# Optimization experiments

Measured on AMD Instinct MI355X. Metric: run time of the kernel, lower is better.

The kernel has to match this reference:

```python
import jax, jax.numpy as jnp
import numpy as np

B, C, T = 8, 128, 8192
SIGMA_MIN = 1e-6

def setup_inputs() -> dict:
    key = jax.random.key(0)
    ks = jax.random.split(key, 9)
    x1 = jax.random.normal(ks[0], (B, C, T), dtype=jnp.float32)
    mu = jax.random.normal(ks[1], (B, C, T), dtype=jnp.float32)
    style = jax.random.normal(ks[2], (B, 192), dtype=jnp.float32)
    t_sample = jax.random.uniform(ks[3], (B, 1, 1), dtype=jnp.float32)
    z = jax.random.normal(ks[4], (B, C, T), dtype=jnp.float32)
    W = jax.random.normal(ks[5], (C, C), dtype=jnp.float32) * (1.0 / np.sqrt(C))
    b_lin = jax.random.normal(ks[6], (C,), dtype=jnp.float32) * 0.01
    prompt_lens = jax.random.randint(ks[7], (B,), 64, T // 4)
    x_lens = jax.random.randint(ks[8], (B,), T // 2, T)
    return {"x1": x1, "mu": mu, "style": style, "t_sample": t_sample, "z": z,
            "W": W, "b_lin": b_lin, "x_lens": x_lens, "prompt_lens": prompt_lens}

def reference(x1, mu, style, t_sample, z, W, b_lin, x_lens, prompt_lens):
    # x1, z: [B, C, T]; t_sample: [B, 1, 1]
    sigma = SIGMA_MIN
    Bb, Cc, Tt = x1.shape
    tpos = jnp.arange(Tt)
    pmask = tpos[None, :] < prompt_lens[:, None]            # [B, T] prompt region
    # flow-matching interpolation
    y = (1.0 - (1.0 - sigma) * t_sample) * z + t_sample * x1
    u = x1 - (1.0 - sigma) * z
    # zero out prompt region of y (prompt copy tensor is unused by the mock estimator)
    y = jnp.where(pmask[:, None, :], 0.0, y)
    # mock estimator: per-timestep Linear over channels
    out = jnp.einsum('bct,dc->bdt', y, W) + b_lin[None, :, None]
    # per-sample MSE over [prompt_lens, x_lens) across all channels, then mean over batch
    lmask = (~pmask) & (tpos[None, :] < x_lens[:, None])     # [B, T]
    diff2 = jnp.square(out - u) * lmask[:, None, :]
    counts = (Cc * jnp.sum(lmask, axis=1)).astype(x1.dtype)  # [B]
    loss = jnp.mean(jnp.sum(diff2, axis=(1, 2)) / counts)
    return loss, out + (1.0 - sigma) * z
```

## Files before the change

kernel.cpp:

```cpp
#include <hip/hip_runtime.h>
#include <hip/hip_bf16.h>

#define BB    8
#define CC    128
#define TLEN  8192
#define TT    32
#define TSPAN 128
#define NB    (BB * (TLEN / TSPAN))

typedef __attribute__((ext_vector_type(8))) short short8;
typedef __attribute__((ext_vector_type(4))) float f32x4;

__device__ __forceinline__ short f2bf(float f) {
    union { float f; unsigned u; } v; v.f = f;
    return (short)((v.u + 0x7FFFu + ((v.u >> 16) & 1u)) >> 16);
}
__device__ __forceinline__ float bf2f(unsigned short h) {
    union { unsigned u; float f; } v; v.u = ((unsigned)h) << 16;
    return v.f;
}
__device__ __forceinline__ int swzY(int t, int c) {
    return c ^ (((t ^ (t >> 3)) & 15) << 3);
}
__device__ __forceinline__ int sfz(int c) {
    return ((c & 3) << 3) | (((c >> 2) & 1) << 2);
}

#define VMWAIT(N) asm volatile("s_waitcnt vmcnt(" #N ")" ::: "memory")
#define SB0 __builtin_amdgcn_sched_barrier(0)

__device__ __forceinline__ void bar_lgkm() {
    asm volatile("s_waitcnt lgkmcnt(0)" ::: "memory");
    __builtin_amdgcn_s_barrier();
}

typedef __attribute__((address_space(1))) const unsigned GU;
typedef __attribute__((address_space(3))) unsigned LU;
__device__ __forceinline__ void glds16(const float* g, const float* l) {
    __builtin_amdgcn_global_load_lds((GU*)g, (LU*)l, 16, 0, 0);
}
__device__ __forceinline__ f32x4 gload(const float* base, unsigned byteoff) {
    f32x4 r;
    asm volatile("global_load_dwordx4 %0, %1, %2"
                 : "=v"(r) : "v"(byteoff), "s"(base));
    return r;
}

__global__ __launch_bounds__(512, 4)
void cfm_fused(const float* __restrict__ x1, const float* __restrict__ tsm,
               const float* __restrict__ z, const float* __restrict__ W,
               const float* __restrict__ blin, const int* __restrict__ xlens,
               const int* __restrict__ plens, float* __restrict__ out)
{
    __shared__ float    zfb[2][CC * TT];
    __shared__ short    ybf[TT][CC];
    __shared__ unsigned zxpk[CC * TT];
    __shared__ float    red[8];

    const int bi = blockIdx.x;
    const int b  = bi & 7;
    const int tb = (bi >> 3) * TSPAN;

    const int tid  = threadIdx.x;
    const int lane = tid & 63;
    const int wid  = tid >> 6;
    const int r15  = lane & 15;
    const int q4   = lane >> 4;

    const float ts  = tsm[b];
    const int   pl  = plens[b];
    const int   xl  = xlens[b];
    const float oms = 0.999999f;
    const float cz  = 1.0f - oms * ts;
    const float cx  = ts;
    const size_t gB = (size_t)b * CC * TLEN;

    short8 af[4];
    {
        const int row = wid * 16 + r15;
        #pragma unroll
        for (int ks = 0; ks < 4; ++ks) {
            const float4 w0 = *reinterpret_cast<const float4*>(W + row * CC + ks * 32 + q4 * 8);
            const float4 w1 = *reinterpret_cast<const float4*>(W + row * CC + ks * 32 + q4 * 8 + 4);
            short8 a;
            a[0] = f2bf(w0.x); a[1] = f2bf(w0.y); a[2] = f2bf(w0.z); a[3] = f2bf(w0.w);
            a[4] = f2bf(w1.x); a[5] = f2bf(w1.y); a[6] = f2bf(w1.z); a[7] = f2bf(w1.w);
            af[ks] = a;
        }
    }
    f32x4 blv = *reinterpret_cast<const f32x4*>(blin + wid * 16 + q4 * 4);
    asm volatile("" :: "v"(blv));

    const int cl  = lane >> 3;
    const int tsw = ((lane & 7) * 4) ^ sfz(cl);
    const int ca  = wid * 16, cb = ca + 8;
    #define STAGEZ(buf, t0k) do {                                             \
        glds16(z + gB + (size_t)(ca + cl) * TLEN + (t0k) + tsw, &zfb[buf][ca * TT]); \
        glds16(z + gB + (size_t)(cb + cl) * TLEN + (t0k) + tsw, &zfb[buf][cb * TT]); \
    } while (0)

    const int rc  = tid >> 2;
    const int t8  = (tid & 3) * 8;
    const int fz  = sfz(rc);
    const unsigned xoff = (unsigned)((gB + (size_t)rc * TLEN) * 4);
    #define XLOAD(xr, t0k) do {                                               \
        xr[0] = gload(x1, xoff + ((t0k) + t8) * 4u);                          \
        xr[1] = gload(x1, xoff + ((t0k) + t8 + 4) * 4u);                      \
    } while (0)

    #define REPACK(buf, t0k, xr) do {                                         \
        const int idx = (rc * TT + t8) ^ fz;                                  \
        const f32x4 za = *reinterpret_cast<const f32x4*>(&zfb[buf][idx]);     \
        const f32x4 zb = *reinterpret_cast<const f32x4*>(&zfb[buf][idx ^ 4]); \
        _Pragma("unroll")                                                     \
        for (int j = 0; j < 4; ++j) {                                         \
            const int ta = t8 + j, tb2 = t8 + 4 + j;                          \
            const float y0 = ((t0k) + ta  < pl) ? 0.0f : cz * za[j] + cx * xr[0][j]; \
            const float y1 = ((t0k) + tb2 < pl) ? 0.0f : cz * zb[j] + cx * xr[1][j]; \
            ybf[ta][swzY(ta, rc)]   = f2bf(y0);                               \
            ybf[tb2][swzY(tb2, rc)] = f2bf(y1);                               \
            zxpk[idx + j]       = ((unsigned)(unsigned short)f2bf(xr[0][j]) << 16) \
                                | (unsigned)(unsigned short)f2bf(za[j]);      \
            zxpk[(idx ^ 4) + j] = ((unsigned)(unsigned short)f2bf(xr[1][j]) << 16) \
                                | (unsigned)(unsigned short)f2bf(zb[j]);      \
        }                                                                     \
    } while (0)

    float lsum = 0.0f;
    #define COMPUTE(t0k) do {                                                 \
        f32x4 acc[2];                                                         \
        acc[0] = (f32x4){0,0,0,0}; acc[1] = (f32x4){0,0,0,0};                 \
        _Pragma("unroll")                                                     \
        for (int ks = 0; ks < 4; ++ks) {                                      \
            _Pragma("unroll")                                                 \
            for (int tt = 0; tt < 2; ++tt) {                                  \
                const int tr = tt * 16 + r15;                                 \
                const short8 ya = *reinterpret_cast<const short8*>(           \
                    &ybf[tr][swzY(tr, ks * 32 + q4 * 8)]);                    \
                acc[tt] = __builtin_amdgcn_mfma_f32_16x16x32_bf16(af[ks], ya, acc[tt], 0, 0, 0); \
            }                                                                 \
        }                                                                     \
        _Pragma("unroll")                                                     \
        for (int rr = 0; rr < 4; ++rr) {                                      \
            const int d = wid * 16 + q4 * 4 + rr;                             \
            float* orow = out + 1 + (size_t)(b * CC + d) * TLEN + (t0k);      \
            const int fd = sfz(d);                                            \
            _Pragma("unroll")                                                 \
            for (int tt = 0; tt < 2; ++tt) {                                  \
                const int tl = tt * 16 + r15;                                 \
                const unsigned p = zxpk[(d * TT + tl) ^ fd];                  \
                const float zv = bf2f((unsigned short)(p & 0xFFFFu));         \
                const float xv = bf2f((unsigned short)(p >> 16));             \
                const float o2 = acc[tt][rr] + blv[rr] + oms * zv;            \
                orow[tl] = o2;                                                \
                const int tg = (t0k) + tl;                                    \
                if ((tg >= pl) & (tg < xl)) { const float df = o2 - xv; lsum += df * df; } \
            }                                                                 \
        }                                                                     \
    } while (0)

    f32x4 x0r[2], x1r[2];
    STAGEZ(0, tb);          XLOAD(x0r, tb);          SB0;
    STAGEZ(1, tb + TT);     XLOAD(x1r, tb + TT);     SB0;

    VMWAIT(4); SB0; bar_lgkm();
    REPACK(0, tb, x0r);
    bar_lgkm();
    STAGEZ(0, tb + 2 * TT); XLOAD(x0r, tb + 2 * TT); SB0;
    COMPUTE(tb);

    VMWAIT(12); SB0; bar_lgkm();
    REPACK(1, tb + TT, x1r);
    bar_lgkm();
    STAGEZ(1, tb + 3 * TT); XLOAD(x1r, tb + 3 * TT); SB0;
    COMPUTE(tb + TT);

    VMWAIT(20); SB0; bar_lgkm();
    REPACK(0, tb + 2 * TT, x0r);
    bar_lgkm();
    COMPUTE(tb + 2 * TT);

    VMWAIT(16); SB0; bar_lgkm();
    REPACK(1, tb + 3 * TT, x1r);
    bar_lgkm();
    COMPUTE(tb + 3 * TT);

    #pragma unroll
    for (int off = 32; off >= 1; off >>= 1) lsum += __shfl_down(lsum, off);
    if (lane == 0) red[wid] = lsum;
    __syncthreads();
    if (tid == 0) {
        float s = 0.0f;
        #pragma unroll
        for (int w = 0; w < 8; ++w) s += red[w];
        atomicAdd(out, s / (1024.0f * (float)(xl - pl)));
    }
}

extern "C" void kernel_launch(void* const* d_in, const int* in_sizes, int n_in,
                              void* d_out, int out_size, void* d_ws, size_t ws_size,
                              hipStream_t stream) {
    const float* x1    = (const float*)d_in[0];
    const float* tsm   = (const float*)d_in[3];
    const float* z     = (const float*)d_in[4];
    const float* W     = (const float*)d_in[5];
    const float* blin  = (const float*)d_in[6];
    const int*   xlens = (const int*)d_in[7];
    const int*   plens = (const int*)d_in[8];
    float* out = (float*)d_out;

    hipMemsetAsync(out, 0, sizeof(float), stream);
    cfm_fused<<<NB, 512, 0, stream>>>(x1, tsm, z, W, blin, xlens, plens, out);
}
```

Baseline: 30.86 us.

## Double-buffer repack tiles to drop barriers and skip x1 loads in prompt

The bf16 y tile and the packed z/x tile in shared memory are now double-buffered, so each stage needs one workgroup barrier instead of two. The barrier is also moved after the next stage's async z and x1 loads are issued. Separately, for time tiles that lie entirely inside the prompt region, the x1 loads are redirected to one clamped address, since those values are zeroed in y and masked out of the loss. This cuts HBM read traffic. The trade-offs are more shared memory per block, which may lower occupancy, and the async LDS writes into the z buffer being issued before other waves are guaranteed to have finished reading it.

```diff
diff --git a/kernel.cpp b/kernel.cpp
--- a/kernel.cpp
+++ b/kernel.cpp
@@ -27,12 +27,8 @@
 }
 
 #define VMWAIT(N) asm volatile("s_waitcnt vmcnt(" #N ")" ::: "memory")
+#define LGKM0     asm volatile("s_waitcnt lgkmcnt(0)" ::: "memory")
 #define SB0 __builtin_amdgcn_sched_barrier(0)
-
-__device__ __forceinline__ void bar_lgkm() {
-    asm volatile("s_waitcnt lgkmcnt(0)" ::: "memory");
-    __builtin_amdgcn_s_barrier();
-}
 
 typedef __attribute__((address_space(1))) const unsigned GU;
 typedef __attribute__((address_space(3))) unsigned LU;
@@ -53,8 +49,8 @@
                const int* __restrict__ plens, float* __restrict__ out)
 {
     __shared__ float    zfb[2][CC * TT];
-    __shared__ short    ybf[TT][CC];
-    __shared__ unsigned zxpk[CC * TT];
+    __shared__ short    ybf[2][TT][CC];
+    __shared__ unsigned zxpk[2][CC * TT];
     __shared__ float    red[8];
 
     const int bi = blockIdx.x;
@@ -74,6 +70,8 @@
     const float cz  = 1.0f - oms * ts;
     const float cx  = ts;
     const size_t gB = (size_t)b * CC * TLEN;
+    const int pclamp = pl & ~(TT - 1);
+    #define XT(t0k) (((t0k) + TT <= pl) ? pclamp : (t0k))
 
     short8 af[4];
     {
@@ -99,9 +97,9 @@
         glds16(z + gB + (size_t)(cb + cl) * TLEN + (t0k) + tsw, &zfb[buf][cb * TT]); \
     } while (0)
 
-    const int rc  = tid >> 2;
-    const int t8  = (tid & 3) * 8;
-    const int fz  = sfz(rc);
+    const int rc = tid >> 2;
+    const int t8 = (tid & 3) * 8;
+    const int fz = sfz(rc);
     const unsigned xoff = (unsigned)((gB + (size_t)rc * TLEN) * 4);
     #define XLOAD(xr, t0k) do {                                               \
         xr[0] = gload(x1, xoff + ((t0k) + t8) * 4u);                          \
@@ -117,17 +115,17 @@
             const int ta = t8 + j, tb2 = t8 + 4 + j;                          \
             const float y0 = ((t0k) + ta  < pl) ? 0.0f : cz * za[j] + cx * xr[0][j]; \
             const float y1 = ((t0k) + tb2 < pl) ? 0.0f : cz * zb[j] + cx * xr[1][j]; \
-            ybf[ta][swzY(ta, rc)]   = f2bf(y0);                               \
-            ybf[tb2][swzY(tb2, rc)] = f2bf(y1);                               \
-            zxpk[idx + j]       = ((unsigned)(unsigned short)f2bf(xr[0][j]) << 16) \
-                                | (unsigned)(unsigned short)f2bf(za[j]);      \
-            zxpk[(idx ^ 4) + j] = ((unsigned)(unsigned short)f2bf(xr[1][j]) << 16) \
-                                | (unsigned)(unsigned short)f2bf(zb[j]);      \
+            ybf[buf][ta][swzY(ta, rc)]   = f2bf(y0);                          \
+            ybf[buf][tb2][swzY(tb2, rc)] = f2bf(y1);                          \
+            zxpk[buf][idx + j]       = ((unsigned)(unsigned short)f2bf(xr[0][j]) << 16) \
+                                     | (unsigned)(unsigned short)f2bf(za[j]); \
+            zxpk[buf][(idx ^ 4) + j] = ((unsigned)(unsigned short)f2bf(xr[1][j]) << 16) \
+                                     | (unsigned)(unsigned short)f2bf(zb[j]); \
         }                                                                     \
     } while (0)
 
     float lsum = 0.0f;
-    #define COMPUTE(t0k) do {                                                 \
+    #define COMPUTE(buf, t0k) do {                                            \
         f32x4 acc[2];                                                         \
         acc[0] = (f32x4){0,0,0,0}; acc[1] = (f32x4){0,0,0,0};                 \
         _Pragma("unroll")                                                     \
@@ -136,7 +134,7 @@
             for (int tt = 0; tt < 2; ++tt) {                                  \
                 const int tr = tt * 16 + r15;                                 \
                 const short8 ya = *reinterpret_cast<const short8*>(           \
-                    &ybf[tr][swzY(tr, ks * 32 + q4 * 8)]);                    \
+                    &ybf[buf][tr][swzY(tr, ks * 32 + q4 * 8)]);               \
                 acc[tt] = __builtin_amdgcn_mfma_f32_16x16x32_bf16(af[ks], ya, acc[tt], 0, 0, 0); \
             }                                                                 \
         }                                                                     \
@@ -148,7 +146,7 @@
             _Pragma("unroll")                                                 \
             for (int tt = 0; tt < 2; ++tt) {                                  \
                 const int tl = tt * 16 + r15;                                 \
-                const unsigned p = zxpk[(d * TT + tl) ^ fd];                  \
+                const unsigned p = zxpk[buf][(d * TT + tl) ^ fd];             \
                 const float zv = bf2f((unsigned short)(p & 0xFFFFu));         \
                 const float xv = bf2f((unsigned short)(p >> 16));             \
                 const float o2 = acc[tt][rr] + blv[rr] + oms * zv;            \
@@ -160,30 +158,34 @@
     } while (0)
 
     f32x4 x0r[2], x1r[2];
-    STAGEZ(0, tb);          XLOAD(x0r, tb);          SB0;
-    STAGEZ(1, tb + TT);     XLOAD(x1r, tb + TT);     SB0;
-
-    VMWAIT(4); SB0; bar_lgkm();
+    STAGEZ(0, tb);          XLOAD(x0r, XT(tb));          SB0;
+    STAGEZ(1, tb + TT);     XLOAD(x1r, XT(tb + TT));     SB0;
+
+    VMWAIT(4); SB0;
     REPACK(0, tb, x0r);
-    bar_lgkm();
-    STAGEZ(0, tb + 2 * TT); XLOAD(x0r, tb + 2 * TT); SB0;
-    COMPUTE(tb);
-
-    VMWAIT(12); SB0; bar_lgkm();
+    LGKM0;
+    STAGEZ(0, tb + 2 * TT); XLOAD(x0r, XT(tb + 2 * TT)); SB0;
+    __builtin_amdgcn_s_barrier();
+    COMPUTE(0, tb);
+
+    VMWAIT(12); SB0;
     REPACK(1, tb + TT, x1r);
-    bar_lgkm();
-    STAGEZ(1, tb + 3 * TT); XLOAD(x1r, tb + 3 * TT); SB0;
-    COMPUTE(tb + TT);
-
-    VMWAIT(20); SB0; bar_lgkm();
+    LGKM0;
+    STAGEZ(1, tb + 3 * TT); XLOAD(x1r, XT(tb + 3 * TT)); SB0;
+    __builtin_amdgcn_s_barrier();
+    COMPUTE(1, tb + TT);
+
+    VMWAIT(20); SB0;
     REPACK(0, tb + 2 * TT, x0r);
-    bar_lgkm();
-    COMPUTE(tb + 2 * TT);
-
-    VMWAIT(16); SB0; bar_lgkm();
+    LGKM0;
+    __builtin_amdgcn_s_barrier();
+    COMPUTE(0, tb + 2 * TT);
+
+    VMWAIT(16); SB0;
     REPACK(1, tb + 3 * TT, x1r);
-    bar_lgkm();
-    COMPUTE(tb + 3 * TT);
+    LGKM0;
+    __builtin_amdgcn_s_barrier();
+    COMPUTE(1, tb + 3 * TT);
 
     #pragma unroll
     for (int off = 32; off >= 1; off >>= 1) lsum += __shfl_down(lsum, off);
```

After: 33.31 us. 8.0% more time.

## Load z directly into registers, halve per-block time span, raise occupancy

Applied to the files above, without the earlier changes.

Each block now covers 64 time steps instead of 128, which doubles the number of blocks. z is no longer staged into shared memory through global_load_lds with double buffering. Each thread instead issues direct dwordx4 loads of x1 and z for both 32-step tiles up front, and shared-memory use drops enough to raise the launch-bounds target to 6 blocks per CU. The goal is more memory-level parallelism and occupancy for this bandwidth-bound kernel, at the cost of a shorter in-block pipeline, more per-block setup (W conversion, bias) and more atomics for the loss.

```diff
diff --git a/kernel.cpp b/kernel.cpp
--- a/kernel.cpp
+++ b/kernel.cpp
@@ -5,7 +5,7 @@
 #define CC    128
 #define TLEN  8192
 #define TT    32
-#define TSPAN 128
+#define TSPAN 64
 #define NB    (BB * (TLEN / TSPAN))
 
 typedef __attribute__((ext_vector_type(8))) short short8;
@@ -27,18 +27,9 @@
 }
 
 #define VMWAIT(N) asm volatile("s_waitcnt vmcnt(" #N ")" ::: "memory")
+#define LGKM0     asm volatile("s_waitcnt lgkmcnt(0)" ::: "memory")
 #define SB0 __builtin_amdgcn_sched_barrier(0)
 
-__device__ __forceinline__ void bar_lgkm() {
-    asm volatile("s_waitcnt lgkmcnt(0)" ::: "memory");
-    __builtin_amdgcn_s_barrier();
-}
-
-typedef __attribute__((address_space(1))) const unsigned GU;
-typedef __attribute__((address_space(3))) unsigned LU;
-__device__ __forceinline__ void glds16(const float* g, const float* l) {
-    __builtin_amdgcn_global_load_lds((GU*)g, (LU*)l, 16, 0, 0);
-}
 __device__ __forceinline__ f32x4 gload(const float* base, unsigned byteoff) {
     f32x4 r;
     asm volatile("global_load_dwordx4 %0, %1, %2"
@@ -46,13 +37,12 @@
     return r;
 }
 
-__global__ __launch_bounds__(512, 4)
+__global__ __launch_bounds__(512, 6)
 void cfm_fused(const float* __restrict__ x1, const float* __restrict__ tsm,
                const float* __restrict__ z, const float* __restrict__ W,
                const float* __restrict__ blin, const int* __restrict__ xlens,
                const int* __restrict__ plens, float* __restrict__ out)
 {
-    __shared__ float    zfb[2][CC * TT];
     __shared__ short    ybf[TT][CC];
     __shared__ unsigned zxpk[CC * TT];
     __shared__ float    red[8];
@@ -90,38 +80,32 @@
     }
     f32x4 blv = *reinterpret_cast<const f32x4*>(blin + wid * 16 + q4 * 4);
     asm volatile("" :: "v"(blv));
+    SB0;
 
-    const int cl  = lane >> 3;
-    const int tsw = ((lane & 7) * 4) ^ sfz(cl);
-    const int ca  = wid * 16, cb = ca + 8;
-    #define STAGEZ(buf, t0k) do {                                             \
-        glds16(z + gB + (size_t)(ca + cl) * TLEN + (t0k) + tsw, &zfb[buf][ca * TT]); \
-        glds16(z + gB + (size_t)(cb + cl) * TLEN + (t0k) + tsw, &zfb[buf][cb * TT]); \
-    } while (0)
+    const int rc = tid >> 2;
+    const int t8 = (tid & 3) * 8;
+    const int fz = sfz(rc);
+    const unsigned rowoff = (unsigned)((gB + (size_t)rc * TLEN) * 4);
 
-    const int rc  = tid >> 2;
-    const int t8  = (tid & 3) * 8;
-    const int fz  = sfz(rc);
-    const unsigned xoff = (unsigned)((gB + (size_t)rc * TLEN) * 4);
-    #define XLOAD(xr, t0k) do {                                               \
-        xr[0] = gload(x1, xoff + ((t0k) + t8) * 4u);                          \
-        xr[1] = gload(x1, xoff + ((t0k) + t8 + 4) * 4u);                      \
-    } while (0)
+    f32x4 xa0, xb0, za0, zb0, xa1, xb1, za1, zb1;
+    xa0 = gload(x1, rowoff + (tb + t8) * 4u);       xb0 = gload(x1, rowoff + (tb + t8 + 4) * 4u);
+    za0 = gload(z,  rowoff + (tb + t8) * 4u);       zb0 = gload(z,  rowoff + (tb + t8 + 4) * 4u);
+    xa1 = gload(x1, rowoff + (tb + TT + t8) * 4u);  xb1 = gload(x1, rowoff + (tb + TT + t8 + 4) * 4u);
+    za1 = gload(z,  rowoff + (tb + TT + t8) * 4u);  zb1 = gload(z,  rowoff + (tb + TT + t8 + 4) * 4u);
+    SB0;
 
-    #define REPACK(buf, t0k, xr) do {                                         \
+    #define REPACK(t0k, xa, xb, za, zb) do {                                  \
         const int idx = (rc * TT + t8) ^ fz;                                  \
-        const f32x4 za = *reinterpret_cast<const f32x4*>(&zfb[buf][idx]);     \
-        const f32x4 zb = *reinterpret_cast<const f32x4*>(&zfb[buf][idx ^ 4]); \
         _Pragma("unroll")                                                     \
         for (int j = 0; j < 4; ++j) {                                         \
             const int ta = t8 + j, tb2 = t8 + 4 + j;                          \
-            const float y0 = ((t0k) + ta  < pl) ? 0.0f : cz * za[j] + cx * xr[0][j]; \
-            const float y1 = ((t0k) + tb2 < pl) ? 0.0f : cz * zb[j] + cx * xr[1][j]; \
+            const float y0 = ((t0k) + ta  < pl) ? 0.0f : cz * za[j] + cx * xa[j]; \
+            const float y1 = ((t0k) + tb2 < pl) ? 0.0f : cz * zb[j] + cx * xb[j]; \
             ybf[ta][swzY(ta, rc)]   = f2bf(y0);                               \
             ybf[tb2][swzY(tb2, rc)] = f2bf(y1);                               \
-            zxpk[idx + j]       = ((unsigned)(unsigned short)f2bf(xr[0][j]) << 16) \
+            zxpk[idx + j]       = ((unsigned)(unsigned short)f2bf(xa[j]) << 16) \
                                 | (unsigned)(unsigned short)f2bf(za[j]);      \
-            zxpk[(idx ^ 4) + j] = ((unsigned)(unsigned short)f2bf(xr[1][j]) << 16) \
+            zxpk[(idx ^ 4) + j] = ((unsigned)(unsigned short)f2bf(xb[j]) << 16) \
                                 | (unsigned)(unsigned short)f2bf(zb[j]);      \
         }                                                                     \
     } while (0)
@@ -159,31 +143,16 @@
         }                                                                     \
     } while (0)
 
-    f32x4 x0r[2], x1r[2];
-    STAGEZ(0, tb);          XLOAD(x0r, tb);          SB0;
-    STAGEZ(1, tb + TT);     XLOAD(x1r, tb + TT);     SB0;
+    VMWAIT(4); SB0;
+    REPACK(tb, xa0, xb0, za0, zb0);
+    LGKM0; __builtin_amdgcn_s_barrier();
+    COMPUTE(tb);
+    __builtin_amdgcn_s_barrier();
 
-    VMWAIT(4); SB0; bar_lgkm();
-    REPACK(0, tb, x0r);
-    bar_lgkm();
-    STAGEZ(0, tb + 2 * TT); XLOAD(x0r, tb + 2 * TT); SB0;
-    COMPUTE(tb);
-
-    VMWAIT(12); SB0; bar_lgkm();
-    REPACK(1, tb + TT, x1r);
-    bar_lgkm();
-    STAGEZ(1, tb + 3 * TT); XLOAD(x1r, tb + 3 * TT); SB0;
+    VMWAIT(8); SB0;
+    REPACK(tb + TT, xa1, xb1, za1, zb1);
+    LGKM0; __builtin_amdgcn_s_barrier();
     COMPUTE(tb + TT);
-
-    VMWAIT(20); SB0; bar_lgkm();
-    REPACK(0, tb + 2 * TT, x0r);
-    bar_lgkm();
-    COMPUTE(tb + 2 * TT);
-
-    VMWAIT(16); SB0; bar_lgkm();
-    REPACK(1, tb + 3 * TT, x1r);
-    bar_lgkm();
-    COMPUTE(tb + 3 * TT);
 
     #pragma unroll
     for (int off = 32; off >= 1; off >>= 1) lsum += __shfl_down(lsum, off);
```

Result: slower. 55.59 us (+80.2%).
